# Performance work log

Measured on AMD Instinct MI355X. Metric: run time of the kernel, lower is better.

Reference implementation:

```python
import jax, jax.numpy as jnp
import numpy as np
from jax import lax

B, S, T = 32, 400, 100
V, OOV = 32000, 100
E, U, AU, GP, ENC = 512, 256, 256, 256, 512


def setup_inputs() -> dict:
    key = jax.random.key(0)
    ks = jax.random.split(key, 24)
    r = lambda k, shp: 0.02 * jax.random.normal(k, shp, dtype=jnp.float32)
    inp = {
        "gt_tokens": jax.random.randint(ks[0], (B, T), 0, V, dtype=jnp.int32),
        "extended_input_tokens": jax.random.randint(ks[1], (B, S), 0, V + OOV, dtype=jnp.int32),
        "enc_output": jax.random.normal(ks[2], (B, S, ENC), dtype=jnp.float32),
        "enc_attn": jax.random.normal(ks[3], (B, S, AU), dtype=jnp.float32),
        "h0": jnp.zeros((B, U), jnp.float32),
        "c0": jnp.zeros((B, U), jnp.float32),
        # learned parameters
        "emb": r(ks[4], (V, E)),
        "lstm_kernel": r(ks[5], (E, 4 * U)),
        "lstm_rec": r(ks[6], (U, 4 * U)),
        "lstm_bias": jnp.zeros((4 * U,), jnp.float32),
        "attn_Wd": r(ks[7], (2 * U, AU)),
        "attn_bd": jnp.zeros((AU,), jnp.float32),
        "attn_Wc": r(ks[8], (1, AU)),
        "attn_Wa": r(ks[9], (AU, 1)),
        "clf_W1": r(ks[10], (U, U)),
        "clf_b1": jnp.zeros((U,), jnp.float32),
        "clf_W2": r(ks[11], (U, V)),
        "clf_b2": jnp.zeros((V,), jnp.float32),
        "gp_Ws": r(ks[12], (2 * U, GP)),
        "gp_Wc": r(ks[13], (ENC, GP)),
        "gp_Wi": r(ks[14], (E, GP)),
        "gp_bi": jnp.zeros((GP,), jnp.float32),
        "gp_Wg": r(ks[15], (GP, 1)),
    }
    return inp


def _decode(gt_tokens, extended_input_tokens, enc_output, enc_attn, h0, c0,
            emb, lstm_kernel, lstm_rec, lstm_bias, attn_Wd, attn_bd, attn_Wc,
            attn_Wa, clf_W1, clf_b1, clf_W2, clf_b2, gp_Ws, gp_Wc, gp_Wi,
            gp_bi, gp_Wg):
    Bn, Sn = extended_input_tokens.shape
    gt_vec = emb[gt_tokens]                      # [B,T,E] teacher-forced inputs
    xs = jnp.swapaxes(gt_vec, 0, 1)              # [T,B,E]
    batch_idx = jnp.arange(Bn)[:, None]

    def step(carry, x):
        h, c, cov = carry                        # [B,U],[B,U],[B,S]
        # single-step LSTM (TF gate order i,f,g,o)
        z = x @ lstm_kernel + h @ lstm_rec + lstm_bias
        i_, f_, g_, o_ = jnp.split(z, 4, axis=-1)
        c = jax.nn.sigmoid(f_) * c + jax.nn.sigmoid(i_) * jnp.tanh(g_)
        h = jax.nn.sigmoid(o_) * jnp.tanh(c)
        dec_state = jnp.concatenate([h, c], axis=1)          # [B,2U]
        # Bahdanau attention with coverage
        dec_attn = dec_state @ attn_Wd + attn_bd             # [B,AU]
        cov_attn = cov[:, :, None] * attn_Wc[0]              # [B,S,AU]
        scores = jnp.tanh(enc_attn + cov_attn + dec_attn[:, None, :]) @ attn_Wa
        a = jax.nn.softmax(scores, axis=1)[:, :, 0]          # [B,S]
        c_vec = jnp.einsum('bse,bs->be', enc_output, a)      # [B,ENC]
        cov_loss = jnp.sum(jnp.minimum(cov, a), axis=1)      # [B]
        cov = cov + a
        # pg: faithful scalar quirk ([0,0,0] of broadcast sum in original)
        g = dec_state[0] @ gp_Ws + c_vec[0] @ gp_Wc + (x[0] @ gp_Wi + gp_bi)
        pg = jax.nn.sigmoid((g @ gp_Wg)[0])
        # vocab distribution, extended with OOV zeros
        vocab_p = jax.nn.softmax((h @ clf_W1 + clf_b1) @ clf_W2 + clf_b2, axis=-1)
        vocab_p = jnp.concatenate([vocab_p, jnp.zeros((Bn, OOV), vocab_p.dtype)], axis=1)
        # copy distribution via scatter-add of attention onto extended ids
        sent_p = jnp.zeros((Bn, V + OOV), a.dtype).at[batch_idx, extended_input_tokens].add(a)
        final = pg * vocab_p + (1.0 - pg) * sent_p           # [B,V+OOV]
        tok = jnp.argmax(final, axis=1).astype(jnp.int32)
        return (h, c, cov), (final, tok, cov_loss)

    cov0 = jnp.zeros((Bn, Sn), jnp.float32)
    _, (probs, seqs, cov_losses) = lax.scan(step, (h0, c0, cov0), xs)
    return (jnp.swapaxes(probs, 0, 1),       # [B,T,V+OOV]
            jnp.swapaxes(seqs, 0, 1),        # [B,T]
            jnp.swapaxes(cov_losses, 0, 1))  # [B,T]


def reference(gt_tokens, extended_input_tokens, enc_output, enc_attn, h0, c0,
              emb, lstm_kernel, lstm_rec, lstm_bias, attn_Wd, attn_bd,
              attn_Wc, attn_Wa, clf_W1, clf_b1, clf_W2, clf_b2, gp_Ws, gp_Wc,
              gp_Wi, gp_bi, gp_Wg):
    return _decode(gt_tokens, extended_input_tokens, enc_output, enc_attn, h0,
                   c0, emb, lstm_kernel, lstm_rec, lstm_bias, attn_Wd,
                   attn_bd, attn_Wc, attn_Wa, clf_W1, clf_b1, clf_W2, clf_b2,
                   gp_Ws, gp_Wc, gp_Wi, gp_bi, gp_Wg)
```

## Files before the change

kernel.cpp:

```cpp
#include <hip/hip_runtime.h>
#include <hip/hip_bf16.h>

#define Bn 32
#define Sn 400
#define Tn 100
#define Vn 32000
#define OOVn 100
#define VEn 32100
#define En 512
#define Un 256
#define AUn 256
#define GPn 256
#define ENCn 512
#define Z4n 1024

typedef __attribute__((ext_vector_type(8))) short bf16x8;
typedef __attribute__((ext_vector_type(4))) float f32x4;
typedef unsigned short ushort_t;
typedef unsigned long long u64;

__device__ __forceinline__ float rcp_f(float x){ return __builtin_amdgcn_rcpf(x); }
__device__ __forceinline__ float tanh_fast(float x){
  float e2 = __expf(2.f*x);
  return 1.f - 2.f*rcp_f(e2 + 1.f);
}
__device__ __forceinline__ float sigmoid_f(float x){ return 1.f/(1.f+__expf(-x)); }
__device__ __forceinline__ ushort_t f2bf(float f){
  unsigned u = __float_as_uint(f);
  unsigned r = (u + 0x7FFFu + ((u>>16)&1u)) >> 16;
  return (ushort_t)r;
}
__device__ __forceinline__ u64 shfl_xor_u64(u64 v, int m){
  unsigned lo = (unsigned)v, hi = (unsigned)(v>>32);
  lo = (unsigned)__shfl_xor((int)lo, m);
  hi = (unsigned)__shfl_xor((int)hi, m);
  return ((u64)hi<<32)|(u64)lo;
}

__device__ __forceinline__ void st_rlx(float* p, float v){
  __hip_atomic_store(p, v, __ATOMIC_RELAXED, __HIP_MEMORY_SCOPE_AGENT);
}
__device__ __forceinline__ float ld_rlx(const float* p){
  return __hip_atomic_load(p, __ATOMIC_RELAXED, __HIP_MEMORY_SCOPE_AGENT);
}
__device__ __forceinline__ void st_flag(unsigned* p, unsigned v){
  __hip_atomic_store(p, v, __ATOMIC_RELAXED, __HIP_MEMORY_SCOPE_AGENT);
}
__device__ __forceinline__ unsigned ld_flag(const unsigned* p){
  return __hip_atomic_load(p, __ATOMIC_RELAXED, __HIP_MEMORY_SCOPE_AGENT);
}


__global__ __launch_bounds__(256) void k_zx(const int* __restrict__ gt,
    const float* __restrict__ emb, const float* __restrict__ Wk,
    const float* __restrict__ bias, float* __restrict__ Zx,
    unsigned* __restrict__ bars, float* __restrict__ covloss){
  __shared__ float As[64][17];
  __shared__ float Bs[16][65];
  __shared__ int tok_lds[64];
  int r0 = blockIdx.x * 64;
  int c0 = blockIdx.y * 64;
  int tid = threadIdx.x;
  int ty = tid >> 4, tx = tid & 15;
  if (blockIdx.x == 0){
    int y = blockIdx.y;
    #pragma unroll
    for (int i = 0; i < 2; ++i){
      int idx = y*512 + i*256 + tid;
      bars[idx] = 0u;
    }
    if (tid < 200) covloss[y*200 + tid] = 0.f;
  }
  if (tid < 64){
    int r = r0 + tid;
    tok_lds[tid] = gt[(r & 31)*Tn + (r >> 5)];
  }
  __syncthreads();
  float acc[4][4] = {};
  for (int k0 = 0; k0 < En; k0 += 16){
    #pragma unroll
    for (int p = 0; p < 4; ++p){
      int row = (tid>>4) + p*16, kk = tid & 15;
      As[row][kk] = emb[(size_t)tok_lds[row]*En + k0 + kk];
    }
    #pragma unroll
    for (int p = 0; p < 4; ++p){
      int kk = (tid>>6) + p*4, cc = tid & 63;
      Bs[kk][cc] = Wk[(size_t)(k0+kk)*Z4n + c0 + cc];
    }
    __syncthreads();
    #pragma unroll
    for (int kk = 0; kk < 16; ++kk){
      float av[4], bv[4];
      #pragma unroll
      for (int i=0;i<4;++i) av[i] = As[ty*4+i][kk];
      #pragma unroll
      for (int j=0;j<4;++j) bv[j] = Bs[kk][tx*4+j];
      #pragma unroll
      for (int i=0;i<4;++i)
        #pragma unroll
        for (int j=0;j<4;++j) acc[i][j] += av[i]*bv[j];
    }
    __syncthreads();
  }
  #pragma unroll
  for (int i=0;i<4;++i){
    int row = r0 + ty*4 + i;
    #pragma unroll
    for (int j=0;j<4;++j){
      int col = c0 + tx*4 + j;
      Zx[(size_t)row*Z4n + col] = acc[i][j] + bias[col];
    }
  }
}


__global__ __launch_bounds__(1024, 1) void k_loop(
    const float* __restrict__ Zx, const float* __restrict__ Wr,
    const float* __restrict__ Wd, const float* __restrict__ bd,
    const float* __restrict__ Wc, const float* __restrict__ Wa,
    const float* __restrict__ enc_attn,
    const float* __restrict__ h0, const float* __restrict__ c0,
    float* __restrict__ h_all, float* __restrict__ decp,
    float* __restrict__ c0_all, float* __restrict__ a_all,
    float* __restrict__ covloss, float* __restrict__ spart,
    unsigned* __restrict__ bars){
  __shared__ float Wr_lds[256*128];
  __shared__ float hfull[Un];
  __shared__ float ppart[8][132];
  __shared__ float zx_lds[128];
  __shared__ float zfull[128];
  __shared__ float hnew[32], cown[32];
  __shared__ float dec_lds[AUn];
  __shared__ float cov_lds[50], sc_lds[50];
  __shared__ float wred[16];
  __shared__ float red8[8];

  const int b = blockIdx.x & 31, k = blockIdx.x >> 5;
  const int tid = threadIdx.x, lane = tid & 63, w = tid >> 6;
  unsigned* flags = bars + b*8*32;
  unsigned* myflag = flags + k*32;

  for (int idx = tid; idx < 256*128; idx += 1024){
    int u = idx >> 7, jl = idx & 127;
    int gcol = 32*k + (jl & 31) + 256*(jl >> 5);
    Wr_lds[idx] = Wr[(size_t)u*Z4n + gcol];
  }
  if (tid < 32) cown[tid] = c0[b*Un + 32*k + tid];
  if (tid < 50) cov_lds[tid] = 0.f;
  const float4 wc4 = *(const float4*)(Wc + lane*4);
  const float4 wa4 = *(const float4*)(Wa + lane*4);
  if (tid < 256) hfull[tid] = h0[b*Un + tid];
  if (tid >= 256 && tid < 384){
    int jl = tid - 256;
    int gcol = 32*k + (jl & 31) + 256*(jl >> 5);
    zx_lds[jl] = Zx[(size_t)(0*Bn + b)*Z4n + gcol];
  }
  __syncthreads();

  {
    int p = tid >> 7, jl = tid & 127;
    float acc = 0.f;
    const float* wr = Wr_lds + (p*32)*128 + jl;
    const float* hb = hfull + p*32;
    #pragma unroll 8
    for (int uu = 0; uu < 32; ++uu) acc += hb[uu]*wr[uu*128];
    ppart[p][jl] = acc;
  }
  __syncthreads();
  if (tid < 128){
    float s = zx_lds[tid];
    #pragma unroll
    for (int q = 0; q < 8; ++q) s += ppart[q][tid];
    zfull[tid] = s;
  }
  __syncthreads();
  if (tid < 32){
    float zi = zfull[tid], zf = zfull[32+tid], zg = zfull[64+tid], zo = zfull[96+tid];
    float cn = sigmoid_f(zf)*cown[tid] + sigmoid_f(zi)*tanhf(zg);
    float hn = sigmoid_f(zo)*tanhf(cn);
    cown[tid] = cn; hnew[tid] = hn;
    int col = 32*k + tid;
    st_rlx(h_all + (size_t)(0*Bn + b)*Un + col, hn);
    if (b == 0) c0_all[0*Un + col] = cn;
  }
  __syncthreads();
  if (tid < 256){
    int c = tid;
    float acc = 0.f;
    const float* wdh = Wd + (size_t)(32*k)*AUn + c;
    #pragma unroll 8
    for (int u = 0; u < 32; ++u) acc += hnew[u]*wdh[(size_t)u*AUn];
    const float* wdc = Wd + (size_t)(Un + 32*k)*AUn + c;
    #pragma unroll 8
    for (int u = 0; u < 32; ++u) acc += cown[u]*wdc[(size_t)u*AUn];
    st_rlx(decp + (size_t)(b*8 + k)*256 + c, acc);
  }
  __syncthreads();
  if (tid == 0) st_flag(myflag, 1u);

  for (int t = 0; t < Tn; ++t){
    const int cur = t & 1, oth = cur ^ 1;
    if (tid < 8){
      while (ld_flag(flags + tid*32) < (unsigned)(t+1))
        __builtin_amdgcn_s_sleep(1);
    }
    __syncthreads();
    if (tid < 256){
      hfull[tid] = ld_rlx(h_all + (size_t)(t*Bn + b)*Un + tid);
    } else if (tid < 512){
      int c = tid - 256;
      float s = bd[c];
      const float* dp = decp + (size_t)cur*(Bn*8*256) + (size_t)(b*8)*256 + c;
      #pragma unroll
      for (int q = 0; q < 8; ++q) s += ld_rlx(dp + q*256);
      dec_lds[c] = s;
    } else if (tid < 520){
      red8[tid-512] = (t > 0) ? ld_rlx(spart + oth*(Bn*8) + b*8 + (tid-512)) : 0.f;
    } else if (tid >= 576 && tid < 704 && t + 1 < Tn){
      int jl = tid - 576;
      int gcol = 32*k + (jl & 31) + 256*(jl >> 5);
      zx_lds[jl] = Zx[(size_t)((t+1)*Bn + b)*Z4n + gcol];
    }
    __syncthreads();
    if (t > 0 && w == 0){
      float pv = (lane < 8) ? red8[lane] : 0.f;
      pv += __shfl_xor(pv, 1); pv += __shfl_xor(pv, 2); pv += __shfl_xor(pv, 4);
      float inv = 1.f / __shfl(pv, 0);
      float clp = 0.f;
      if (lane < 50){
        float aa = sc_lds[lane] * inv;
        float co = cov_lds[lane];
        a_all[(size_t)((t-1)*Bn + b)*Sn + 50*k + lane] = aa;
        clp = fminf(co, aa);
        cov_lds[lane] = co + aa;
      }
      #pragma unroll
      for (int m = 1; m < 64; m <<= 1) clp += __shfl_xor(clp, m);
      if (lane == 0) atomicAdd(&covloss[b*Tn + (t-1)], clp);
    }
    {
      int p = tid >> 7, jl = tid & 127;
      float acc = 0.f;
      const float* wr = Wr_lds + (p*32)*128 + jl;
      const float* hb = hfull + p*32;
      #pragma unroll 8
      for (int uu = 0; uu < 32; ++uu) acc += hb[uu]*wr[uu*128];
      ppart[p][jl] = acc;
    }
    __syncthreads();
    if (tid < 128 && t + 1 < Tn){
      float s = zx_lds[tid];
      #pragma unroll
      for (int q = 0; q < 8; ++q) s += ppart[q][tid];
      zfull[tid] = s;
    }
    __syncthreads();
    if (tid < 32 && t + 1 < Tn){
      float zi = zfull[tid], zf = zfull[32+tid], zg = zfull[64+tid], zo = zfull[96+tid];
      float cn = sigmoid_f(zf)*cown[tid] + sigmoid_f(zi)*tanhf(zg);
      float hn = sigmoid_f(zo)*tanhf(cn);
      cown[tid] = cn; hnew[tid] = hn;
      int col = 32*k + tid;
      st_rlx(h_all + (size_t)((t+1)*Bn + b)*Un + col, hn);
      if (b == 0) c0_all[(t+1)*Un + col] = cn;
    }
    __syncthreads();
    if (w < 4){
      if (t + 1 < Tn){
        int c = tid;
        float acc = 0.f;
        const float* wdh = Wd + (size_t)(32*k)*AUn + c;
        #pragma unroll 8
        for (int u = 0; u < 32; ++u) acc += hnew[u]*wdh[(size_t)u*AUn];
        const float* wdc = Wd + (size_t)(Un + 32*k)*AUn + c;
        #pragma unroll 8
        for (int u = 0; u < 32; ++u) acc += cown[u]*wdc[(size_t)u*AUn];
        st_rlx(decp + (size_t)oth*(Bn*8*256) + (size_t)(b*8 + k)*256 + c, acc);
      }
    } else {
      const float4 da = *(const float4*)(dec_lds + lane*4);
      float wsum = 0.f;
      for (int sl = w - 4; sl < 50; sl += 12){
        float cvv = cov_lds[sl];
        const float4 e = *(const float4*)(enc_attn + ((size_t)(b*Sn + 50*k + sl))*AUn + lane*4);
        float psc = tanh_fast(e.x + cvv*wc4.x + da.x)*wa4.x
                  + tanh_fast(e.y + cvv*wc4.y + da.y)*wa4.y
                  + tanh_fast(e.z + cvv*wc4.z + da.z)*wa4.z
                  + tanh_fast(e.w + cvv*wc4.w + da.w)*wa4.w;
        #pragma unroll
        for (int m = 1; m < 64; m <<= 1) psc += __shfl_xor(psc, m);
        if (lane == 0){
          float ev = __expf(psc);
          sc_lds[sl] = ev;
          wsum += ev;
        }
      }
      if (lane == 0) wred[w] = wsum;
    }
    __syncthreads();
    if (tid == 0){
      float S = 0.f;
      #pragma unroll
      for (int q = 4; q < 16; ++q) S += wred[q];
      st_rlx(spart + cur*(Bn*8) + b*8 + k, S);
    }
    __syncthreads();
    if (tid == 0) st_flag(myflag, (unsigned)(t + 2));
  }

  if (tid < 8){
    while (ld_flag(flags + tid*32) < (unsigned)(Tn + 1))
      __builtin_amdgcn_s_sleep(1);
  }
  __syncthreads();
  if (tid < 8) red8[tid] = ld_rlx(spart + ((Tn-1)&1)*(Bn*8) + b*8 + tid);
  __syncthreads();
  if (w == 0){
    float pv = (lane < 8) ? red8[lane] : 0.f;
    pv += __shfl_xor(pv, 1); pv += __shfl_xor(pv, 2); pv += __shfl_xor(pv, 4);
    float inv = 1.f / __shfl(pv, 0);
    float clp = 0.f;
    if (lane < 50){
      float aa = sc_lds[lane] * inv;
      float co = cov_lds[lane];
      a_all[(size_t)((Tn-1)*Bn + b)*Sn + 50*k + lane] = aa;
      clp = fminf(co, aa);
    }
    #pragma unroll
    for (int m = 1; m < 64; m <<= 1) clp += __shfl_xor(clp, m);
    if (lane == 0) atomicAdd(&covloss[b*Tn + (Tn-1)], clp);
  }
}


__global__ __launch_bounds__(256) void k_misc(
    const float* __restrict__ W2, ushort_t* __restrict__ W2T,
    const float* __restrict__ h_all, const float* __restrict__ W1,
    const float* __restrict__ b1, ushort_t* __restrict__ hid,
    const int* __restrict__ gt, const float* __restrict__ emb,
    const float* __restrict__ gpWi, const float* __restrict__ gpbi,
    const float* __restrict__ a_all, const float* __restrict__ enc_out,
    const float* __restrict__ c0_all, const float* __restrict__ gpWs,
    const float* __restrict__ gpWc, const float* __restrict__ gpWg,
    float* __restrict__ pg, float* __restrict__ Ssum, u64* __restrict__ amax){
  __shared__ __align__(16) char sbuf[32768];
  int bid = blockIdx.x, tid = threadIdx.x;
  if (bid < 2000){
    if (bid < 13){
      int idx = bid*256 + tid;
      if (idx < 3200) Ssum[idx] = 0.f;
    } else if (bid < 26){
      int idx = (bid-13)*256 + tid;
      if (idx < 3200) amax[idx] = 0ull;
    }
    float (*tile)[65] = (float(*)[65])sbuf;
    int n0 = (bid % 500) * 64, k0 = (bid / 500) * 64;
    int tx = tid & 63, ty4 = tid >> 6;
    #pragma unroll
    for (int i = 0; i < 16; ++i){
      int kk = ty4 + i*4;
      tile[kk][tx] = W2[(size_t)(k0+kk)*Vn + n0 + tx];
    }
    __syncthreads();
    #pragma unroll
    for (int i = 0; i < 16; ++i){
      int n = ty4 + i*4;
      W2T[(size_t)(n0+n)*Un + k0 + tx] = f2bf(tile[tx][n]);
    }
  } else if (bid < 2100){
    float* hl = (float*)sbuf;
    int t = bid - 2000;
    for (int i = tid; i < Bn*Un; i += 256) hl[i] = h_all[(size_t)t*Bn*Un + i];
    __syncthreads();
    int j = tid;
    float bj = b1[j];
    float acc[32];
    #pragma unroll
    for (int r = 0; r < 32; ++r) acc[r] = bj;
    for (int u = 0; u < Un; ++u){
      float wv = W1[u*Un + j];
      #pragma unroll
      for (int r = 0; r < 32; ++r) acc[r] += hl[r*Un + u]*wv;
    }
    #pragma unroll
    for (int r = 0; r < 32; ++r) hid[(size_t)(t*Bn + r)*Un + j] = f2bf(acc[r]);
  } else {
    int t = bid - 2100;
    float* al  = (float*)sbuf;
    float* cv  = al + 400;
    float* xl  = cv + 512;
    float* red = xl + 512;
    for (int s = tid; s < Sn; s += 256) al[s] = a_all[(size_t)(t*Bn)*Sn + s];
    for (int i = tid; i < En; i += 256) xl[i] = emb[(size_t)gt[t]*En + i];
    __syncthreads();
    for (int e = tid; e < ENCn; e += 256){
      float acc = 0.f;
      for (int s = 0; s < Sn; ++s) acc += enc_out[(size_t)s*ENCn + e]*al[s];
      cv[e] = acc;
    }
    __syncthreads();
    int j = tid;
    float g = gpbi[j];
    for (int u = 0; u < En; ++u) g += xl[u]*gpWi[u*GPn + j];
    const float* h0r = h_all + (size_t)t*Bn*Un;
    const float* c0r = c0_all + t*Un;
    for (int u = 0; u < Un; ++u) g += h0r[u]*gpWs[u*GPn + j];
    for (int u = 0; u < Un; ++u) g += c0r[u]*gpWs[(Un+u)*GPn + j];
    for (int e = 0; e < ENCn; ++e) g += cv[e]*gpWc[e*GPn + j];
    float v = g * gpWg[j];
    int lane = tid & 63, wv2 = tid >> 6;
    #pragma unroll
    for (int m = 1; m < 64; m <<= 1) v += __shfl_xor(v, m);
    if (lane == 0) red[wv2] = v;
    __syncthreads();
    if (tid == 0) pg[t] = 1.f/(1.f+__expf(-(red[0]+red[1]+red[2]+red[3])));
  }
}

__global__ __launch_bounds__(512) void k_gemm(const ushort_t* __restrict__ A,
    const ushort_t* __restrict__ Bw, const float* __restrict__ b2,
    float* __restrict__ Ssum, u64* __restrict__ amax, const float* __restrict__ pg,
    float* __restrict__ probs, int mode){
  int r0 = blockIdx.x * 128;
  int n0 = blockIdx.y * 256;
  int tid = threadIdx.x;
  if (mode == 1 && n0 >= Vn){
    for (int idx = tid; idx < 128*OOVn; idx += 512){
      int i = idx/OOVn, vv = idx%OOVn;
      int r = r0+i; int tt = r>>5, bb = r&31;
      probs[(size_t)(bb*Tn+tt)*VEn + Vn + vv] = 0.f;
    }
    return;
  }
  __shared__ ushort_t Bs[64*264];
  int lane = tid & 63, w = tid >> 6;
  bf16x8 af[8];
  {
    const ushort_t* ar = A + (size_t)(r0 + w*16 + (lane&15))*Un + (lane>>4)*8;
    #pragma unroll
    for (int kk = 0; kk < 8; ++kk) af[kk] = *(const bf16x8*)(ar + kk*32);
  }
  f32x4 acc[16];
  #pragma unroll
  for (int i = 0; i < 16; ++i) acc[i] = (f32x4){0.f,0.f,0.f,0.f};

  for (int nsub = 0; nsub < 4; ++nsub){
    __syncthreads();
    {
      const ushort_t* gb = Bw + (size_t)(n0 + nsub*64)*Un;
      #pragma unroll
      for (int i = 0; i < 4; ++i){
        int chunk = tid + i*512;
        int rr = chunk >> 5, cc = chunk & 31;
        uint4 d = *(const uint4*)(gb + rr*Un + cc*8);
        *(uint4*)(Bs + rr*264 + cc*8) = d;
      }
    }
    __syncthreads();
    #pragma unroll
    for (int kk = 0; kk < 8; ++kk){
      #pragma unroll
      for (int ntl = 0; ntl < 4; ++ntl){
        bf16x8 bf = *(const bf16x8*)(Bs + (ntl*16 + (lane&15))*264 + kk*32 + (lane>>4)*8);
        acc[nsub*4+ntl] = __builtin_amdgcn_mfma_f32_16x16x32_bf16(af[kk], bf, acc[nsub*4+ntl], 0, 0, 0);
      }
    }
  }

  int rowloc = w*16 + (lane>>4)*4;
  if (mode == 0){
    float rs[4] = {0.f,0.f,0.f,0.f};
    #pragma unroll
    for (int nt = 0; nt < 16; ++nt){
      int v = n0 + (nt>>2)*64 + (nt&3)*16 + (lane&15);
      float bb = b2[v];
      #pragma unroll
      for (int i = 0; i < 4; ++i) rs[i] += __expf(acc[nt][i] + bb);
    }
    #pragma unroll
    for (int m = 1; m < 16; m <<= 1)
      #pragma unroll
      for (int i = 0; i < 4; ++i) rs[i] += __shfl_xor(rs[i], m);
    if ((lane&15) == 0)
      #pragma unroll
      for (int i = 0; i < 4; ++i) atomicAdd(&Ssum[r0+rowloc+i], rs[i]);
  } else {
    float sc[4]; size_t obase[4];
    #pragma unroll
    for (int i = 0; i < 4; ++i){
      int r = r0+rowloc+i; int tt = r>>5, bb = r&31;
      sc[i] = pg[tt] / Ssum[r];
      obase[i] = (size_t)(bb*Tn+tt)*VEn;
    }
    u64 pm[4] = {0,0,0,0};
    #pragma unroll
    for (int nt = 0; nt < 16; ++nt){
      int v = n0 + (nt>>2)*64 + (nt&3)*16 + (lane&15);
      float bb = b2[v];
      #pragma unroll
      for (int i = 0; i < 4; ++i){
        float val = __expf(acc[nt][i] + bb) * sc[i];
        __builtin_nontemporal_store(val, &probs[obase[i] + v]);
        u64 p = ((u64)__float_as_uint(val)<<32) | (u64)(0xFFFFFFFFu - (unsigned)v);
        pm[i] = p > pm[i] ? p : pm[i];
      }
    }
    #pragma unroll
    for (int m = 1; m < 16; m <<= 1)
      #pragma unroll
      for (int i = 0; i < 4; ++i){
        u64 o = shfl_xor_u64(pm[i], m);
        pm[i] = o > pm[i] ? o : pm[i];
      }
    if ((lane&15) == 0)
      #pragma unroll
      for (int i = 0; i < 4; ++i) atomicMax(&amax[r0+rowloc+i], pm[i]);
  }
}

__global__ __launch_bounds__(256) void k_scatter(const int* __restrict__ ext,
    const float* __restrict__ a_all, const float* __restrict__ pg,
    float* __restrict__ probs, const u64* __restrict__ amax,
    float* __restrict__ seqs){
  __shared__ int   hkey[1024];
  __shared__ float hval[1024];
  __shared__ u64   wmax[4];
  int r = blockIdx.x; int t = r>>5, b = r&31;
  float c1 = 1.f - pg[t];
  int tid = threadIdx.x;
  #pragma unroll
  for (int i = 0; i < 4; ++i){
    hkey[tid + i*256] = -1;
    hval[tid + i*256] = 0.f;
  }
  __syncthreads();
  for (int s = tid; s < Sn; s += 256){
    int key = ext[b*Sn + s];
    float v = c1 * a_all[(size_t)r*Sn + s];
    unsigned h = ((unsigned)key * 2654435761u) >> 22;
    for (;;){
      int old = atomicCAS(&hkey[h], -1, key);
      if (old == -1 || old == key) break;
      h = (h + 1) & 1023;
    }
    atomicAdd(&hval[h], v);
  }
  __syncthreads();
  size_t obase = (size_t)(b*Tn + t)*VEn;
  u64 pm = 0;
  #pragma unroll
  for (int i = 0; i < 4; ++i){
    int slot = tid + i*256;
    int tk = hkey[slot];
    if (tk >= 0){
      float nv = probs[obase + tk] + hval[slot];
      probs[obase + tk] = nv;
      u64 p = ((u64)__float_as_uint(nv)<<32) | (u64)(0xFFFFFFFFu - (unsigned)tk);
      pm = p > pm ? p : pm;
    }
  }
  #pragma unroll
  for (int m = 1; m < 64; m <<= 1){
    u64 o = shfl_xor_u64(pm, m);
    pm = o > pm ? o : pm;
  }
  int lane = tid & 63, w = tid >> 6;
  if (lane == 0) wmax[w] = pm;
  __syncthreads();
  if (tid == 0){
    u64 mm = amax[r];
    #pragma unroll
    for (int q = 0; q < 4; ++q) mm = wmax[q] > mm ? wmax[q] : mm;
    unsigned tk = 0xFFFFFFFFu - (unsigned)(mm & 0xFFFFFFFFull);
    seqs[b*Tn + t] = (float)tk;
  }
}


extern "C" void kernel_launch(void* const* d_in, const int* in_sizes, int n_in,
                              void* d_out, int out_size, void* d_ws, size_t ws_size,
                              hipStream_t stream){
  (void)in_sizes; (void)n_in; (void)out_size; (void)ws_size;
  const int*   gt       = (const int*)d_in[0];
  const int*   ext      = (const int*)d_in[1];
  const float* enc_out  = (const float*)d_in[2];
  const float* enc_attn = (const float*)d_in[3];
  const float* h0       = (const float*)d_in[4];
  const float* c0       = (const float*)d_in[5];
  const float* emb      = (const float*)d_in[6];
  const float* Wk       = (const float*)d_in[7];
  const float* Wr       = (const float*)d_in[8];
  const float* lb       = (const float*)d_in[9];
  const float* Wd       = (const float*)d_in[10];
  const float* bd       = (const float*)d_in[11];
  const float* Wc       = (const float*)d_in[12];
  const float* Wa       = (const float*)d_in[13];
  const float* W1       = (const float*)d_in[14];
  const float* b1       = (const float*)d_in[15];
  const float* W2       = (const float*)d_in[16];
  const float* b2       = (const float*)d_in[17];
  const float* gpWs     = (const float*)d_in[18];
  const float* gpWc     = (const float*)d_in[19];
  const float* gpWi     = (const float*)d_in[20];
  const float* gpbi     = (const float*)d_in[21];
  const float* gpWg     = (const float*)d_in[22];

  float* probs   = (float*)d_out;
  float* seqs    = probs + (size_t)Bn*Tn*VEn;
  float* covloss = seqs + Bn*Tn;

  char* wp = (char*)d_ws;
  auto carve = [&](size_t bytes)->void*{
    void* p = (void*)wp; wp += (bytes + 255) & ~(size_t)255; return p;
  };
  float*    Zx      = (float*)carve((size_t)3200*Z4n*4);
  float*    h_all   = (float*)carve((size_t)Tn*Bn*Un*4);
  float*    decp    = (float*)carve((size_t)2*Bn*8*256*4);
  float*    c0_all  = (float*)carve((size_t)Tn*Un*4);
  float*    a_all   = (float*)carve((size_t)3200*Sn*4);
  ushort_t* hid_bf  = (ushort_t*)carve((size_t)3200*Un*2);
  ushort_t* W2T     = (ushort_t*)carve((size_t)Vn*Un*2);
  float*    Ssum    = (float*)carve((size_t)3200*4);
  u64*      amax    = (u64*)carve((size_t)3200*8);
  float*    pg      = (float*)carve((size_t)Tn*4);
  float*    spart   = (float*)carve((size_t)2*Bn*8*4);
  unsigned* bars    = (unsigned*)carve((size_t)Bn*8*32*4);

  k_zx  <<<dim3(50,16), 256, 0, stream>>>(gt, emb, Wk, lb, Zx, bars, covloss);

  k_loop<<<256, 1024, 0, stream>>>(Zx, Wr, Wd, bd, Wc, Wa, enc_attn,
                                   h0, c0, h_all, decp, c0_all,
                                   a_all, covloss, spart, bars);

  k_misc<<<2200, 256, 0, stream>>>(W2, W2T, h_all, W1, b1, hid_bf,
                                   gt, emb, gpWi, gpbi, a_all, enc_out,
                                   c0_all, gpWs, gpWc, gpWg, pg, Ssum, amax);
  k_gemm<<<dim3(25,125), 512, 0, stream>>>(hid_bf, W2T, b2, Ssum, amax, pg, probs, 0);
  k_gemm<<<dim3(25,126), 512, 0, stream>>>(hid_bf, W2T, b2, Ssum, amax, pg, probs, 1);
  k_scatter<<<3200, 256, 0, stream>>>(ext, a_all, pg, probs, amax, seqs);
}
```

Before: 1.227 ms.

## Keep full W2 column tile resident in LDS and loop blocks over row chunks

Each GEMM block now loads a 256-column slice of the transposed classifier weight into shared memory once and iterates over 12–13 row chunks of 128, rather than reloading weight slices for every 128-row tile. The grid shrinks from 25x125 to 2x125 blocks, with one block per CU via launch bounds and about 135KB of LDS. Zeroing of the OOV probability columns moves from the extra GEMM column-block into the scatter kernel. The aim is to cut repeated weight traffic and LDS staging, at the cost of only 250 blocks, which may leave the 256 CUs underfilled and removes latency hiding across blocks.

```diff
diff --git a/kernel.cpp b/kernel.cpp
--- a/kernel.cpp
+++ b/kernel.cpp
@@ -418,105 +418,98 @@
   }
 }
 
-__global__ __launch_bounds__(512) void k_gemm(const ushort_t* __restrict__ A,
+__global__ __launch_bounds__(512, 1) void k_gemm(const ushort_t* __restrict__ A,
     const ushort_t* __restrict__ Bw, const float* __restrict__ b2,
     float* __restrict__ Ssum, u64* __restrict__ amax, const float* __restrict__ pg,
     float* __restrict__ probs, int mode){
-  int r0 = blockIdx.x * 128;
+  __shared__ ushort_t Bs[256*264];
+  int gx = blockIdx.x;
   int n0 = blockIdx.y * 256;
   int tid = threadIdx.x;
-  if (mode == 1 && n0 >= Vn){
-    for (int idx = tid; idx < 128*OOVn; idx += 512){
-      int i = idx/OOVn, vv = idx%OOVn;
-      int r = r0+i; int tt = r>>5, bb = r&31;
-      probs[(size_t)(bb*Tn+tt)*VEn + Vn + vv] = 0.f;
-    }
-    return;
-  }
-  __shared__ ushort_t Bs[64*264];
   int lane = tid & 63, w = tid >> 6;
-  bf16x8 af[8];
   {
-    const ushort_t* ar = A + (size_t)(r0 + w*16 + (lane&15))*Un + (lane>>4)*8;
-    #pragma unroll
-    for (int kk = 0; kk < 8; ++kk) af[kk] = *(const bf16x8*)(ar + kk*32);
-  }
-  f32x4 acc[16];
-  #pragma unroll
-  for (int i = 0; i < 16; ++i) acc[i] = (f32x4){0.f,0.f,0.f,0.f};
-
-  for (int nsub = 0; nsub < 4; ++nsub){
-    __syncthreads();
+    int rr = tid >> 1, half = (tid & 1) * 128;
+    const ushort_t* gb = Bw + (size_t)(n0 + rr)*Un + half;
+    ushort_t* lb = Bs + rr*264 + half;
+    #pragma unroll
+    for (int j = 0; j < 16; ++j)
+      *((uint4*)lb + j) = *((const uint4*)gb + j);
+  }
+  __syncthreads();
+
+  int cbase = (gx == 0) ? 0 : 13;
+  int nch   = (gx == 0) ? 13 : 12;
+  float bb[4];
+  for (int ci = 0; ci < nch; ++ci){
+    int r0 = (cbase + ci) * 128;
+    bf16x8 af[8];
     {
-      const ushort_t* gb = Bw + (size_t)(n0 + nsub*64)*Un;
+      const ushort_t* ar = A + (size_t)(r0 + w*16 + (lane&15))*Un + (lane>>4)*8;
+      #pragma unroll
+      for (int kk = 0; kk < 8; ++kk) af[kk] = *(const bf16x8*)(ar + kk*32);
+    }
+    f32x4 acc[16];
+    #pragma unroll
+    for (int i = 0; i < 16; ++i) acc[i] = (f32x4){0.f,0.f,0.f,0.f};
+    #pragma unroll
+    for (int kk = 0; kk < 8; ++kk){
+      #pragma unroll
+      for (int nt = 0; nt < 16; ++nt){
+        bf16x8 bf = *(const bf16x8*)(Bs + (nt*16 + (lane&15))*264 + kk*32 + (lane>>4)*8);
+        acc[nt] = __builtin_amdgcn_mfma_f32_16x16x32_bf16(af[kk], bf, acc[nt], 0, 0, 0);
+      }
+    }
+    int rowloc = w*16 + (lane>>4)*4;
+    if (mode == 0){
+      float rs[4] = {0.f,0.f,0.f,0.f};
+      #pragma unroll
+      for (int nt = 0; nt < 16; ++nt){
+        int v = n0 + nt*16 + (lane&15);
+        float b2v = b2[v];
+        #pragma unroll
+        for (int i = 0; i < 4; ++i) rs[i] += __expf(acc[nt][i] + b2v);
+      }
+      #pragma unroll
+      for (int m = 1; m < 16; m <<= 1)
+        #pragma unroll
+        for (int i = 0; i < 4; ++i) rs[i] += __shfl_xor(rs[i], m);
+      if ((lane&15) == 0)
+        #pragma unroll
+        for (int i = 0; i < 4; ++i) atomicAdd(&Ssum[r0+rowloc+i], rs[i]);
+    } else {
+      float sc[4]; size_t obase[4];
       #pragma unroll
       for (int i = 0; i < 4; ++i){
-        int chunk = tid + i*512;
-        int rr = chunk >> 5, cc = chunk & 31;
-        uint4 d = *(const uint4*)(gb + rr*Un + cc*8);
-        *(uint4*)(Bs + rr*264 + cc*8) = d;
+        int r = r0+rowloc+i; int tt = r>>5, bbx = r&31;
+        sc[i] = pg[tt] / Ssum[r];
+        obase[i] = (size_t)(bbx*Tn+tt)*VEn;
       }
-    }
-    __syncthreads();
-    #pragma unroll
-    for (int kk = 0; kk < 8; ++kk){
-      #pragma unroll
-      for (int ntl = 0; ntl < 4; ++ntl){
-        bf16x8 bf = *(const bf16x8*)(Bs + (ntl*16 + (lane&15))*264 + kk*32 + (lane>>4)*8);
-        acc[nsub*4+ntl] = __builtin_amdgcn_mfma_f32_16x16x32_bf16(af[kk], bf, acc[nsub*4+ntl], 0, 0, 0);
+      u64 pm[4] = {0,0,0,0};
+      #pragma unroll
+      for (int nt = 0; nt < 16; ++nt){
+        int v = n0 + nt*16 + (lane&15);
+        float b2v = b2[v];
+        #pragma unroll
+        for (int i = 0; i < 4; ++i){
+          float val = __expf(acc[nt][i] + b2v) * sc[i];
+          __builtin_nontemporal_store(val, &probs[obase[i] + v]);
+          u64 p = ((u64)__float_as_uint(val)<<32) | (u64)(0xFFFFFFFFu - (unsigned)v);
+          pm[i] = p > pm[i] ? p : pm[i];
+        }
       }
-    }
-  }
-
-  int rowloc = w*16 + (lane>>4)*4;
-  if (mode == 0){
-    float rs[4] = {0.f,0.f,0.f,0.f};
-    #pragma unroll
-    for (int nt = 0; nt < 16; ++nt){
-      int v = n0 + (nt>>2)*64 + (nt&3)*16 + (lane&15);
-      float bb = b2[v];
-      #pragma unroll
-      for (int i = 0; i < 4; ++i) rs[i] += __expf(acc[nt][i] + bb);
-    }
-    #pragma unroll
-    for (int m = 1; m < 16; m <<= 1)
-      #pragma unroll
-      for (int i = 0; i < 4; ++i) rs[i] += __shfl_xor(rs[i], m);
-    if ((lane&15) == 0)
-      #pragma unroll
-      for (int i = 0; i < 4; ++i) atomicAdd(&Ssum[r0+rowloc+i], rs[i]);
-  } else {
-    float sc[4]; size_t obase[4];
-    #pragma unroll
-    for (int i = 0; i < 4; ++i){
-      int r = r0+rowloc+i; int tt = r>>5, bb = r&31;
-      sc[i] = pg[tt] / Ssum[r];
-      obase[i] = (size_t)(bb*Tn+tt)*VEn;
-    }
-    u64 pm[4] = {0,0,0,0};
-    #pragma unroll
-    for (int nt = 0; nt < 16; ++nt){
-      int v = n0 + (nt>>2)*64 + (nt&3)*16 + (lane&15);
-      float bb = b2[v];
-      #pragma unroll
-      for (int i = 0; i < 4; ++i){
-        float val = __expf(acc[nt][i] + bb) * sc[i];
-        __builtin_nontemporal_store(val, &probs[obase[i] + v]);
-        u64 p = ((u64)__float_as_uint(val)<<32) | (u64)(0xFFFFFFFFu - (unsigned)v);
-        pm[i] = p > pm[i] ? p : pm[i];
-      }
-    }
-    #pragma unroll
-    for (int m = 1; m < 16; m <<= 1)
-      #pragma unroll
-      for (int i = 0; i < 4; ++i){
-        u64 o = shfl_xor_u64(pm[i], m);
-        pm[i] = o > pm[i] ? o : pm[i];
-      }
-    if ((lane&15) == 0)
-      #pragma unroll
-      for (int i = 0; i < 4; ++i) atomicMax(&amax[r0+rowloc+i], pm[i]);
-  }
+      #pragma unroll
+      for (int m = 1; m < 16; m <<= 1)
+        #pragma unroll
+        for (int i = 0; i < 4; ++i){
+          u64 o = shfl_xor_u64(pm[i], m);
+          pm[i] = o > pm[i] ? o : pm[i];
+        }
+      if ((lane&15) == 0)
+        #pragma unroll
+        for (int i = 0; i < 4; ++i) atomicMax(&amax[r0+rowloc+i], pm[i]);
+    }
+  }
+  (void)bb;
 }
 
 __global__ __launch_bounds__(256) void k_scatter(const int* __restrict__ ext,
@@ -534,6 +527,8 @@
     hkey[tid + i*256] = -1;
     hval[tid + i*256] = 0.f;
   }
+  size_t obase = (size_t)(b*Tn + t)*VEn;
+  if (tid < OOVn) probs[obase + Vn + tid] = 0.f;
   __syncthreads();
   for (int s = tid; s < Sn; s += 256){
     int key = ext[b*Sn + s];
@@ -547,7 +542,6 @@
     atomicAdd(&hval[h], v);
   }
   __syncthreads();
-  size_t obase = (size_t)(b*Tn + t)*VEn;
   u64 pm = 0;
   #pragma unroll
   for (int i = 0; i < 4; ++i){
@@ -636,7 +630,7 @@
   k_misc<<<2200, 256, 0, stream>>>(W2, W2T, h_all, W1, b1, hid_bf,
                                    gt, emb, gpWi, gpbi, a_all, enc_out,
                                    c0_all, gpWs, gpWc, gpWg, pg, Ssum, amax);
-  k_gemm<<<dim3(25,125), 512, 0, stream>>>(hid_bf, W2T, b2, Ssum, amax, pg, probs, 0);
-  k_gemm<<<dim3(25,126), 512, 0, stream>>>(hid_bf, W2T, b2, Ssum, amax, pg, probs, 1);
+  k_gemm<<<dim3(2,125), 512, 0, stream>>>(hid_bf, W2T, b2, Ssum, amax, pg, probs, 0);
+  k_gemm<<<dim3(2,125), 512, 0, stream>>>(hid_bf, W2T, b2, Ssum, amax, pg, probs, 1);
   k_scatter<<<3200, 256, 0, stream>>>(ext, a_all, pg, probs, amax, seqs);
 }
```

After: 1.182 ms. -3.6%, faster.
